# Performance work log

Hardware: AMD Instinct MI355X
Metric: run time of the kernel (lower is better)

Reference implementation:

```python
import jax, jax.numpy as jnp
import numpy as np

B = 2
NUM_CLS = 20
NUM_DIM = 256
H = W = 448
FH = FW = 28
K_TOP = 25


def _l2norm(x, eps=1e-12):
    # matches torch F.normalize(dim=1): x / max(||x||, eps); zero rows stay zero
    return x / jnp.maximum(jnp.linalg.norm(x, axis=-1, keepdims=True), eps)


def setup_inputs():
    key = jax.random.key(0)
    k1, k2, k3, k4 = jax.random.split(key, 4)
    fmap = jax.random.normal(k1, (B, NUM_DIM, FH, FW), jnp.float32)
    cam = jax.random.uniform(k2, (B, NUM_CLS, H, W), jnp.float32)
    cls_label = jax.random.randint(k3, (B, NUM_CLS), 0, 2).astype(jnp.float32)
    proj_weight = jax.random.normal(k4, (NUM_CLS, NUM_DIM), jnp.float32) * 0.02
    feature_contrast = jnp.zeros((NUM_CLS, NUM_DIM), jnp.float32)
    return {"fmap": fmap, "cam": cam, "cls_label": cls_label,
            "proj_weight": proj_weight, "feature_contrast": feature_contrast,
            "hig_thre": 0.7, "low_thre": 0.25, "bg_thre": 0.5}


def _forward(fmap, cam, cls_label, proj_weight, feature_contrast, hig_thre, low_thre, bg_thre):
    b, c, h, w = cam.shape
    d = fmap.shape[1]
    dt = fmap.dtype

    # ---- pseudo-label generation (vectorized over b,h,w) ----
    valid_cam = cls_label[:, :, None, None] * cam                       # [B,C,H,W]
    top2_v, top2_i = jax.lax.top_k(jnp.moveaxis(valid_cam, 1, -1), 2)   # [B,H,W,2]
    top1, second = top2_v[..., 0], top2_v[..., 1]
    pseudo = top2_i[..., 0] + 1
    pseudo = jnp.where(top1 < hig_thre, 255, pseudo)
    pseudo = jnp.where(top1 < low_thre, 0, pseudo)
    pseudo = jnp.where(top1 < bg_thre, 0, pseudo)
    pseudo = jnp.where((top1 - second < 0.3) & (top1 > hig_thre), 255, pseudo)

    # ---- upsample features (bilinear, align_corners=False) ----
    fmap_up = jax.image.resize(fmap, (b, d, h, w), 'bilinear')
    fmap_flat = fmap_up.reshape(b, d, h * w)                            # [B,D,HW]
    pseudo_flat = pseudo.reshape(b, h * w)                              # [B,HW]

    # ---- per-class features, both branches computed densely then selected ----
    cls_ids = jnp.arange(c) + 1
    mask = (pseudo_flat[:, None, :] == cls_ids[None, :, None]).astype(dt)  # [B,C,HW]
    counts = mask.sum(-1)                                                  # [B,C]
    feat_mask = jnp.einsum('bcp,bdp->bcd', mask, fmap_flat) / jnp.maximum(counts, 1.0)[:, :, None]
    _, top_idx = jax.lax.top_k(valid_cam.reshape(b, c, h * w), K_TOP)      # [B,C,25]
    gathered = jnp.take_along_axis(fmap_flat[:, None, :, :], top_idx[:, :, None, :], axis=-1)  # [B,C,D,25]
    feat_topk = gathered.mean(-1)                                          # [B,C,D]
    present = cls_label > 0.5                                              # [B,C] bool
    fsm = jnp.where((counts == 0.0)[:, :, None], feat_topk, feat_mask) * present[:, :, None]

    eye_f = jnp.eye(c, dtype=dt)
    eye_b = jnp.eye(c, dtype=bool)

    # ---- sequential per-sample loop (EMA memory bank carried across batch) ----
    def step(carry, xs):
        fc, loss_cls, loss_ccf = carry
        fsm_i, present_i = xs                                    # [C,D], [C]
        fsm_n = _l2norm(fsm_i)
        fc_n = _l2norm(jax.lax.stop_gradient(fc))
        cos = jnp.clip(jnp.abs(fsm_n @ fc_n.T), 1e-5, 1.0 - 1e-5)  # [C,C]
        ident = jnp.diag(present_i.astype(dt))
        loss_ccf = loss_ccf - (ident * jnp.log(cos) + (1.0 - ident) * jnp.log1p(-cos)).mean()
        off_max = jnp.where(eye_b, -jnp.inf, cos).max(axis=1)      # max over j != c
        qualify = present_i & (off_max < 0.6)                      # [C] bool
        p = jax.nn.softmax(fsm_i @ proj_weight.T, axis=-1)         # [C,C]
        logp = jnp.maximum(jnp.log(p), -100.0)
        log1mp = jnp.maximum(jnp.log1p(-p), -100.0)
        term = -(eye_f * logp + (1.0 - eye_f) * log1mp).mean(axis=-1)  # BCE(softmax, onehot) per class
        loss_cls = loss_cls + jnp.sum(jnp.where(qualify, term, 0.0))
        n = qualify.sum().astype(dt)
        loss_cls = jnp.where(n > 0, loss_cls / jnp.maximum(n, 1.0), loss_cls)
        fc = jnp.where(qualify[:, None], 0.95 * fc + 0.05 * jax.lax.stop_gradient(fsm_i), fc)
        return (fc, loss_cls, loss_ccf), None

    zero = jnp.asarray(0.0, dt)
    (_, loss_cls, loss_ccf), _ = jax.lax.scan(step, (feature_contrast, zero, zero), (fsm, present))
    return loss_ccf + loss_cls


def reference(fmap, cam, cls_label, proj_weight, feature_contrast, hig_thre, low_thre, bg_thre):
    return _forward(fmap, cam, cls_label, proj_weight, feature_contrast, hig_thre, low_thre, bg_thre)
```

## Files before the change

kernel.cpp:

```cpp
#include <hip/hip_runtime.h>
#include <cstdint>

#define HW 200704
#define IMG_W 448
#define NCLS 20
#define NDIM 256
#define NB2 784
#define LK 260

#define ASYNC_COPY4(gp, lp)                                                    \
  __builtin_amdgcn_global_load_lds(                                            \
      (const __attribute__((address_space(1))) void*)(gp),                     \
      (__attribute__((address_space(3))) void*)(lp), 4, 0, 0)

__global__ __launch_bounds__(256) void k_front(const float* __restrict__ fmap,
                                               float* __restrict__ fmapT,
                                               const float* __restrict__ cam,
                                               const float* __restrict__ cls_label,
                                               const float* __restrict__ hig_p,
                                               const float* __restrict__ low_p,
                                               const float* __restrict__ bg_p,
                                               float* __restrict__ W) {
  __shared__ float sT[NCLS][256];
  int tid = threadIdx.x;

  if (blockIdx.x >= 2 * NB2) {
    float (*tile)[33] = (float (*)[33]) & sT[0][0];
    int blk = blockIdx.x - 2 * NB2;
    int b = blk / 200;
    int t = blk % 200;
    int dT = t / 25, sT2 = t % 25;
    int ty = tid >> 5, tx = tid & 31;
#pragma unroll
    for (int r = 0; r < 4; ++r) {
      int d = dT * 32 + ty + r * 8;
      int s = sT2 * 32 + tx;
      if (s < 784) tile[ty + r * 8][tx] = fmap[((size_t)(b * 256 + d)) * 784 + s];
    }
    __syncthreads();
#pragma unroll
    for (int r = 0; r < 4; ++r) {
      int s = sT2 * 32 + ty + r * 8;
      int d = dT * 32 + tx;
      if (s < 784) fmapT[((size_t)(b * 784 + s)) * 256 + d] = tile[tx][ty + r * 8];
    }
    return;
  }

  int b = blockIdx.x / NB2;
  int blkInB = blockIdx.x % NB2;
  int pix0 = blkInB * 256;
  int wave = tid >> 6, lane = tid & 63;

  bool pres = (lane < NCLS) && (cls_label[b * NCLS + lane] != 0.0f);
  unsigned long long pm = __ballot(pres);
  unsigned mask = (unsigned)(pm & 0xFFFFFu);
  int np = __popc(mask);
  const float* camb = cam + (size_t)b * NCLS * HW + pix0 + wave * 64 + lane;

  {
    unsigned m = mask;
    for (int k = 0; k < np; ++k) {
      int c = __builtin_ctz(m); m &= m - 1u;
      ASYNC_COPY4(camb + (size_t)c * HW, &sT[k][wave * 64]);
    }
  }
  __builtin_amdgcn_s_waitcnt(0);

  float top1 = -1.0f, sec = -1.0f;
  int cls1 = 0;
  {
    unsigned m = mask;
    for (int k = 0; k < np; ++k) {
      int c = __builtin_ctz(m); m &= m - 1u;
      float x = sT[k][tid];
      bool gt = x > top1;
      sec = gt ? top1 : fmaxf(sec, fminf(x, top1));
      cls1 = gt ? c : cls1;
      top1 = gt ? x : top1;
    }
  }
  if (np < NCLS) sec = fmaxf(sec, 0.0f);
  float hig = hig_p[0], low = low_p[0], bg = bg_p[0];
  int pix = pix0 + tid;
  int ps = cls1 + 1;
  if (top1 < hig) ps = 255;
  if (top1 < low) ps = 0;
  if (top1 < bg)  ps = 0;
  if ((top1 - sec < 0.3f) && (top1 > hig)) ps = 255;
  if (ps >= 1 && ps <= NCLS) {
    int cls = ps - 1;
    int y = pix / IMG_W, x = pix % IMG_W;
    float sy = (y + 0.5f) * 0.0625f - 0.5f; sy = fminf(fmaxf(sy, 0.0f), 27.0f);
    float sx = (x + 0.5f) * 0.0625f - 0.5f; sx = fminf(fmaxf(sx, 0.0f), 27.0f);
    int fy0 = (int)sy, fx0 = (int)sx;
    int fy1 = min(fy0 + 1, 27), fx1 = min(fx0 + 1, 27);
    float wy = sy - (float)fy0, wx = sx - (float)fx0;
    float* Wb = W + (size_t)(b * NCLS + cls) * 784;
    atomicAdd(&Wb[fy0 * 28 + fx0], (1.0f - wy) * (1.0f - wx));
    atomicAdd(&Wb[fy0 * 28 + fx1], (1.0f - wy) * wx);
    atomicAdd(&Wb[fy1 * 28 + fx0], wy * (1.0f - wx));
    atomicAdd(&Wb[fy1 * 28 + fx1], wy * wx);
  }
}

__global__ __launch_bounds__(512) void k_feat(const float* __restrict__ fmapT,
                                              const float* __restrict__ cam,
                                              const float* __restrict__ Wg,
                                              const float* __restrict__ cls_label,
                                              float* __restrict__ P,
                                              float* __restrict__ S,
                                              float* __restrict__ cntW) {
  __shared__ float sW[784];
  __shared__ float sH[2][256];
  __shared__ float sRed[8];
  __shared__ float sCntf;
  __shared__ float wv[8]; __shared__ int wi[8];
  __shared__ float selV; __shared__ int selI;
  __shared__ int sTop[25];
  int bc = blockIdx.x >> 2, part = blockIdx.x & 3;
  int b = bc / NCLS;
  int tid = threadIdx.x;
  int dim = tid & 255, h = tid >> 8;
  if (cls_label[bc] == 0.0f) return;

  for (int s = tid; s < 784; s += 512) sW[s] = Wg[(size_t)bc * 784 + s];
  __syncthreads();
  {
    float cs = sW[tid >= 512 ? 0 : tid];
    cs = (tid < 512) ? sW[tid] : 0.0f;
    if (tid < 272) cs += sW[tid + 512];
    for (int off = 32; off > 0; off >>= 1) cs += __shfl_xor(cs, off, 64);
    if ((tid & 63) == 0) sRed[tid >> 6] = cs;
    __syncthreads();
    if (tid == 0) {
      float s = 0.0f;
      for (int w = 0; w < 8; ++w) s += sRed[w];
      sCntf = s;
    }
    __syncthreads();
  }
  float cntf = sCntf;
  const float* fT = fmapT + (size_t)b * 784 * 256;

  if (cntf > 0.0f) {
    int s0 = part * 196;
    if (h == 0) {
      float a0 = 0.0f, a1 = 0.0f;
      for (int s = s0; s < s0 + 196; s += 4) {
        a0 += sW[s]     * fT[(size_t)(s)     * 256 + dim];
        a1 += sW[s + 1] * fT[(size_t)(s + 1) * 256 + dim];
      }
      sH[0][dim] = a0 + a1;
    } else {
      float a2 = 0.0f, a3 = 0.0f;
      for (int s = s0; s < s0 + 196; s += 4) {
        a2 += sW[s + 2] * fT[(size_t)(s + 2) * 256 + dim];
        a3 += sW[s + 3] * fT[(size_t)(s + 3) * 256 + dim];
      }
      sH[1][dim] = a2 + a3;
    }
    __syncthreads();
    if (tid < 256)
      P[(size_t)(bc * 4 + part) * 256 + tid] = sH[0][tid] + sH[1][tid];
    if (part == 0 && tid == 0) cntW[bc] = cntf;
  } else if (part == 0) {
    if (tid == 0) cntW[bc] = 0.0f;
    const float* camc = cam + (size_t)bc * HW;
    float lastV = 3.0e38f; int lastI = -1;
    for (int r = 0; r < 25; ++r) {
      float bv = -1.0e30f; int bi = 0x7fffffff;
      for (int p = tid; p < HW; p += 512) {
        float vv2 = camc[p];
        if (((vv2 < lastV) || (vv2 == lastV && p > lastI)) &&
            ((vv2 > bv) || (vv2 == bv && p < bi))) { bv = vv2; bi = p; }
      }
      for (int off = 32; off > 0; off >>= 1) {
        float ov = __shfl_xor(bv, off, 64);
        int   oi = __shfl_xor(bi, off, 64);
        if (ov > bv || (ov == bv && oi < bi)) { bv = ov; bi = oi; }
      }
      if ((tid & 63) == 0) { wv[tid >> 6] = bv; wi[tid >> 6] = bi; }
      __syncthreads();
      if (tid == 0) {
        for (int w = 1; w < 8; ++w)
          if (wv[w] > bv || (wv[w] == bv && wi[w] < bi)) { bv = wv[w]; bi = wi[w]; }
        selV = bv; selI = bi; sTop[r] = bi;
      }
      __syncthreads();
      lastV = selV; lastI = selI;
    }
    if (tid < 256) {
      float at = 0.0f;
      for (int r = 0; r < 25; ++r) {
        int p = sTop[r];
        int y = p / IMG_W, x = p % IMG_W;
        float sy = (y + 0.5f) * 0.0625f - 0.5f; sy = fminf(fmaxf(sy, 0.0f), 27.0f);
        float sx = (x + 0.5f) * 0.0625f - 0.5f; sx = fminf(fmaxf(sx, 0.0f), 27.0f);
        int fy0 = (int)sy, fx0 = (int)sx;
        int fy1 = min(fy0 + 1, 27), fx1 = min(fx0 + 1, 27);
        float wy = sy - (float)fy0, wx = sx - (float)fx0;
        at += (1.0f - wy) * (1.0f - wx) * fT[(size_t)(fy0 * 28 + fx0) * 256 + tid]
            + (1.0f - wy) * wx          * fT[(size_t)(fy0 * 28 + fx1) * 256 + tid]
            + wy          * (1.0f - wx) * fT[(size_t)(fy1 * 28 + fx0) * 256 + tid]
            + wy          * wx          * fT[(size_t)(fy1 * 28 + fx1) * 256 + tid];
      }
      S[(size_t)bc * 256 + tid] = at * (1.0f / 25.0f);
    }
  }
}

__global__ __launch_bounds__(256) void k_pre(const float* __restrict__ P,
                                             const float* __restrict__ S,
                                             const float* __restrict__ cntW,
                                             const float* __restrict__ cls_label,
                                             const float* __restrict__ proj_w,
                                             const float* __restrict__ fc_init,
                                             float* __restrict__ BCEg,
                                             float* __restrict__ COS0,
                                             float* __restrict__ COS1V) {
  __shared__ float sOwn[LK];
  __shared__ float sFc[NCLS * LK], sPw[NCLS * LK];
  __shared__ float sF0[NCLS * LK], sFv[NCLS * LK];
  __shared__ float sLog[NCLS];
  __shared__ float sNC[NCLS], sNCv[NCLS];
  __shared__ int   sZC[NCLS], sZCv[NCLS];
  __shared__ float sNI[1]; __shared__ int sZI[1];
  int tid = threadIdx.x;
  int b = blockIdx.x / NCLS, i = blockIdx.x % NCLS;

  for (int idx = tid; idx < NCLS * NDIM; idx += 256) {
    int r = idx >> 8, d = idx & 255;
    sFc[r * LK + d] = fc_init[idx];
    sPw[r * LK + d] = proj_w[idx];
  }
  {
    int bc = b * NCLS + i, d = tid;
    float v = 0.0f;
    if (cls_label[bc] != 0.0f) {
      float c = cntW[bc];
      if (c > 0.0f) {
        const float* p = P + (size_t)bc * 1024 + d;
        v = ((p[0] + p[256]) + (p[512] + p[768])) / fmaxf(c, 1.0f);
      } else {
        v = S[(size_t)bc * 256 + d];
      }
    }
    sOwn[d] = v;
  }
  if (b == 1) {
    for (int idx = tid; idx < NCLS * NDIM; idx += 256) {
      int bc = idx >> 8, d = idx & 255;
      float v = 0.0f;
      if (cls_label[bc] != 0.0f) {
        float c = cntW[bc];
        if (c > 0.0f) {
          const float* p = P + (size_t)bc * 1024 + d;
          v = ((p[0] + p[256]) + (p[512] + p[768])) / fmaxf(c, 1.0f);
        } else {
          v = S[(size_t)bc * 256 + d];
        }
      }
      sF0[bc * LK + d] = v;
    }
  }
  __syncthreads();
  if (b == 1) {
    for (int idx = tid; idx < NCLS * NDIM; idx += 256) {
      int r = idx >> 8, d = idx & 255;
      sFv[r * LK + d] = 0.95f * sFc[r * LK + d] + 0.05f * sF0[r * LK + d];
    }
    __syncthreads();
  }

  {
    int g = tid >> 3, sub = tid & 7;
    if (g <= 20) {
      const float* row = (g < 20) ? &sFc[g * LK] : sOwn;
      float a0 = 0.0f, a1 = 0.0f, a2 = 0.0f, a3 = 0.0f;
      int d0 = sub * 32;
#pragma unroll
      for (int d = d0; d < d0 + 32; d += 8) {
        float4 x = *(const float4*)&row[d];
        float4 y = *(const float4*)&row[d + 4];
        a0 += x.x * x.x + x.y * x.y;
        a1 += x.z * x.z + x.w * x.w;
        a2 += y.x * y.x + y.y * y.y;
        a3 += y.z * y.z + y.w * y.w;
      }
      float s = (a0 + a1) + (a2 + a3);
      s += __shfl_xor(s, 1, 64);
      s += __shfl_xor(s, 2, 64);
      s += __shfl_xor(s, 4, 64);
      if (sub == 0) {
        if (g < 20) { sNC[g] = fmaxf(sqrtf(s), 1e-12f); sZC[g] = (s == 0.0f); }
        else        { sNI[0] = fmaxf(sqrtf(s), 1e-12f); sZI[0] = (s == 0.0f); }
      }
    }
  }
  __syncthreads();
  if (b == 1) {
    int g = tid >> 3, sub = tid & 7;
    if (g < 20) {
      const float* row = &sFv[g * LK];
      float a0 = 0.0f, a1 = 0.0f, a2 = 0.0f, a3 = 0.0f;
      int d0 = sub * 32;
#pragma unroll
      for (int d = d0; d < d0 + 32; d += 8) {
        float4 x = *(const float4*)&row[d];
        float4 y = *(const float4*)&row[d + 4];
        a0 += x.x * x.x + x.y * x.y;
        a1 += x.z * x.z + x.w * x.w;
        a2 += y.x * y.x + y.y * y.y;
        a3 += y.z * y.z + y.w * y.w;
      }
      float s = (a0 + a1) + (a2 + a3);
      s += __shfl_xor(s, 1, 64);
      s += __shfl_xor(s, 2, 64);
      s += __shfl_xor(s, 4, 64);
      if (sub == 0) { sNCv[g] = fmaxf(sqrtf(s), 1e-12f); sZCv[g] = (s == 0.0f); }
    }
    __syncthreads();
  }

  if (tid < NCLS) {
    const float* ra = sOwn;
    const float* rb = &sPw[tid * LK];
    float a0 = 0, a1 = 0, a2 = 0, a3 = 0, a4 = 0, a5 = 0, a6 = 0, a7 = 0;
    for (int d = 0; d < 256; d += 16) {
      float4 x0 = *(const float4*)&ra[d],      y0 = *(const float4*)&rb[d];
      float4 x1 = *(const float4*)&ra[d + 4],  y1 = *(const float4*)&rb[d + 4];
      float4 x2 = *(const float4*)&ra[d + 8],  y2 = *(const float4*)&rb[d + 8];
      float4 x3 = *(const float4*)&ra[d + 12], y3 = *(const float4*)&rb[d + 12];
      a0 += x0.x * y0.x + x0.y * y0.y;  a1 += x0.z * y0.z + x0.w * y0.w;
      a2 += x1.x * y1.x + x1.y * y1.y;  a3 += x1.z * y1.z + x1.w * y1.w;
      a4 += x2.x * y2.x + x2.y * y2.y;  a5 += x2.z * y2.z + x2.w * y2.w;
      a6 += x3.x * y3.x + x3.y * y3.y;  a7 += x3.z * y3.z + x3.w * y3.w;
    }
    sLog[tid] = ((a0 + a1) + (a2 + a3)) + ((a4 + a5) + (a6 + a7));
  }
  __syncthreads();

  if (tid < 32) {
    int jj = tid;
    float l = (jj < NCLS) ? sLog[jj] : -3.0e38f;
    float m = l;
#pragma unroll
    for (int off = 1; off < 32; off <<= 1) m = fmaxf(m, __shfl_xor(m, off, 64));
    float e = (jj < NCLS) ? expf(l - m) : 0.0f;
    float sS = e;
#pragma unroll
    for (int off = 1; off < 32; off <<= 1) sS += __shfl_xor(sS, off, 64);
    float term = 0.0f;
    if (jj < NCLS) {
      float p = e / sS;
      term = (jj == i) ? fmaxf(logf(p), -100.0f) : fmaxf(log1pf(-p), -100.0f);
    }
#pragma unroll
    for (int off = 1; off < 32; off <<= 1) term += __shfl_xor(term, off, 64);
    if (jj == 0) BCEg[b * NCLS + i] = -term / 20.0f;
  }
  if (tid >= 64 && tid < 64 + 2 * NCLS) {
    int j = (tid - 64) >> 1, sub = tid & 1;
    float c0;
    if (sZI[0] || sZC[j]) c0 = 0.0f;
    else {
      const float* ra = sOwn;
      const float* rb = &sFc[j * LK];
      float a0 = 0.0f, a1 = 0.0f, a2 = 0.0f, a3 = 0.0f;
      int d0 = sub * 128;
      for (int d = d0; d < d0 + 128; d += 8) {
        float4 x  = *(const float4*)&ra[d];
        float4 y  = *(const float4*)&rb[d];
        float4 x2 = *(const float4*)&ra[d + 4];
        float4 y2 = *(const float4*)&rb[d + 4];
        a0 += x.x * y.x + x.y * y.y;
        a1 += x.z * y.z + x.w * y.w;
        a2 += x2.x * y2.x + x2.y * y2.y;
        a3 += x2.z * y2.z + x2.w * y2.w;
      }
      float acc = (a0 + a1) + (a2 + a3);
      acc += __shfl_xor(acc, 1, 64);
      c0 = fabsf(acc / (sNI[0] * sNC[j]));
    }
    if (sub == 0) {
      float cv = fminf(fmaxf(c0, 1e-5f), 1.0f - 1e-5f);
      if (b == 0) COS0[i * NCLS + j] = cv;
      else        COS1V[i * NCLS + j] = cv;
    }
  }
  if (b == 1 && tid >= 128 && tid < 128 + 2 * NCLS) {
    int j = (tid - 128) >> 1, sub = tid & 1;
    float c0;
    if (sZI[0] || sZCv[j]) c0 = 0.0f;
    else {
      const float* ra = sOwn;
      const float* rb = &sFv[j * LK];
      float a0 = 0.0f, a1 = 0.0f, a2 = 0.0f, a3 = 0.0f;
      int d0 = sub * 128;
      for (int d = d0; d < d0 + 128; d += 8) {
        float4 x  = *(const float4*)&ra[d];
        float4 y  = *(const float4*)&rb[d];
        float4 x2 = *(const float4*)&ra[d + 4];
        float4 y2 = *(const float4*)&rb[d + 4];
        a0 += x.x * y.x + x.y * y.y;
        a1 += x.z * y.z + x.w * y.w;
        a2 += x2.x * y2.x + x2.y * y2.y;
        a3 += x2.z * y2.z + x2.w * y2.w;
      }
      float acc = (a0 + a1) + (a2 + a3);
      acc += __shfl_xor(acc, 1, 64);
      c0 = fabsf(acc / (sNI[0] * sNCv[j]));
    }
    if (sub == 0)
      COS1V[400 + i * NCLS + j] = fminf(fmaxf(c0, 1e-5f), 1.0f - 1e-5f);
  }
}

__global__ __launch_bounds__(1024) void k_final(const float* __restrict__ BCEg,
                                                const float* __restrict__ COS0,
                                                const float* __restrict__ COS1V,
                                                const float* __restrict__ cls_label,
                                                float* __restrict__ out) {
  __shared__ float sCos[400];
  __shared__ float sBCE[2][NCLS], sRow[NCLS];
  __shared__ int   sQual[NCLS];
  __shared__ float sPres[2][NCLS];
  __shared__ float sScal[2];
  int tid = threadIdx.x;

  if (tid < 400) sCos[tid] = COS0[tid];
  if (tid < 40) { sBCE[tid / NCLS][tid % NCLS] = BCEg[tid];
                  sPres[tid / NCLS][tid % NCLS] = cls_label[tid]; }
  if (tid == 0) { sScal[0] = 0.0f; sScal[1] = 0.0f; }
  __syncthreads();

  for (int b = 0; b < 2; ++b) {
    if (b == 1) {
      if (tid < 400) {
        int j = tid % NCLS;
        sCos[tid] = sQual[j] ? COS1V[400 + tid] : COS1V[tid];
      }
      __syncthreads();
    }
    {
      int i = tid >> 5, jj = tid & 31;
      if (i < NCLS) {
        float pres = (sPres[b][i] > 0.5f) ? 1.0f : 0.0f;
        float contrib = 0.0f, omv = -3.0e38f;
        if (jj < NCLS) {
          float c0 = sCos[i * NCLS + jj];
          float ident = (jj == i) ? pres : 0.0f;
          contrib = ident * logf(c0) + (1.0f - ident) * log1pf(-c0);
          if (jj != i) omv = c0;
        }
#pragma unroll
        for (int off = 1; off < 32; off <<= 1) {
          contrib += __shfl_xor(contrib, off, 64);
          omv = fmaxf(omv, __shfl_xor(omv, off, 64));
        }
        if (jj == 0) { sRow[i] = contrib; sQual[i] = (pres > 0.5f && omv < 0.6f) ? 1 : 0; }
      }
    }
    __syncthreads();
    if (tid == 0) {
      float s = 0.0f;
      for (int r = 0; r < NCLS; ++r) s += sRow[r];
      sScal[0] -= s / 400.0f;
      float add = 0.0f; int nq = 0;
      for (int r = 0; r < NCLS; ++r) if (sQual[r]) { add += sBCE[b][r]; nq++; }
      float lc = sScal[1] + add;
      if (nq > 0) lc = lc / fmaxf((float)nq, 1.0f);
      sScal[1] = lc;
    }
    __syncthreads();
  }
  if (tid == 0) out[0] = sScal[0] + sScal[1];
}

extern "C" void kernel_launch(void* const* d_in, const int* in_sizes, int n_in,
                              void* d_out, int out_size, void* d_ws, size_t ws_size,
                              hipStream_t stream) {
  const float* fmap      = (const float*)d_in[0];
  const float* cam       = (const float*)d_in[1];
  const float* cls_label = (const float*)d_in[2];
  const float* proj_w    = (const float*)d_in[3];
  const float* fc_init   = (const float*)d_in[4];
  const float* hig       = (const float*)d_in[5];
  const float* low       = (const float*)d_in[6];
  const float* bg        = (const float*)d_in[7];
  float* out = (float*)d_out;

  char* ws = (char*)d_ws;
  float* W     = (float*)(ws);
  float* cntW  = (float*)(ws + 125440);
  float* P     = (float*)(ws + 125600);
  float* S     = (float*)(ws + 289440);
  float* fmapT = (float*)(ws + 330400);
  float* BCEg  = (float*)(ws + 1936032);
  float* COS0v = (float*)(ws + 1936192);
  float* COS1V = (float*)(ws + 1937792);

  hipMemsetAsync(ws, 0, 125440, stream);
  k_front<<<2 * NB2 + 400,  256, 0, stream>>>(fmap, fmapT, cam, cls_label,
                                              hig, low, bg, W);
  k_feat <<<          160,  512, 0, stream>>>(fmapT, cam, W, cls_label, P, S, cntW);
  k_pre  <<<   2 * NCLS,    256, 0, stream>>>(P, S, cntW, cls_label, proj_w,
                                              fc_init, BCEg, COS0v, COS1V);
  k_final<<<            1, 1024, 0, stream>>>(BCEg, COS0v, COS1V, cls_label, out);
}
```

Measured before the change: 121.0 us.

## Merge feature, pre and final kernels into one launch with atomic tickets

Fuses k_feat, k_pre and k_final into a single 200-block kernel. The last 40 blocks preload their constant tables, then spin on an atomic ticket counter until the 160 feature blocks finish. The final reduction runs in whichever pre block increments the second ticket last. This removes two kernel launches and their inter-kernel gaps. It depends on all 200 blocks being co-resident, since a waiting block would otherwise deadlock, and the pre blocks now use 512 threads, which raises their shared-memory and register footprint.

```diff
diff --git a/kernel.cpp b/kernel.cpp
--- a/kernel.cpp
+++ b/kernel.cpp
@@ -104,121 +104,127 @@
   }
 }
 
-__global__ __launch_bounds__(512) void k_feat(const float* __restrict__ fmapT,
-                                              const float* __restrict__ cam,
-                                              const float* __restrict__ Wg,
-                                              const float* __restrict__ cls_label,
-                                              float* __restrict__ P,
-                                              float* __restrict__ S,
-                                              float* __restrict__ cntW) {
-  __shared__ float sW[784];
-  __shared__ float sH[2][256];
-  __shared__ float sRed[8];
-  __shared__ float sCntf;
-  __shared__ float wv[8]; __shared__ int wi[8];
-  __shared__ float selV; __shared__ int selI;
-  __shared__ int sTop[25];
-  int bc = blockIdx.x >> 2, part = blockIdx.x & 3;
-  int b = bc / NCLS;
-  int tid = threadIdx.x;
-  int dim = tid & 255, h = tid >> 8;
-  if (cls_label[bc] == 0.0f) return;
-
-  for (int s = tid; s < 784; s += 512) sW[s] = Wg[(size_t)bc * 784 + s];
-  __syncthreads();
-  {
-    float cs = sW[tid >= 512 ? 0 : tid];
-    cs = (tid < 512) ? sW[tid] : 0.0f;
-    if (tid < 272) cs += sW[tid + 512];
-    for (int off = 32; off > 0; off >>= 1) cs += __shfl_xor(cs, off, 64);
-    if ((tid & 63) == 0) sRed[tid >> 6] = cs;
-    __syncthreads();
-    if (tid == 0) {
-      float s = 0.0f;
-      for (int w = 0; w < 8; ++w) s += sRed[w];
-      sCntf = s;
-    }
-    __syncthreads();
-  }
-  float cntf = sCntf;
-  const float* fT = fmapT + (size_t)b * 784 * 256;
-
-  if (cntf > 0.0f) {
-    int s0 = part * 196;
-    if (h == 0) {
-      float a0 = 0.0f, a1 = 0.0f;
-      for (int s = s0; s < s0 + 196; s += 4) {
-        a0 += sW[s]     * fT[(size_t)(s)     * 256 + dim];
-        a1 += sW[s + 1] * fT[(size_t)(s + 1) * 256 + dim];
-      }
-      sH[0][dim] = a0 + a1;
-    } else {
-      float a2 = 0.0f, a3 = 0.0f;
-      for (int s = s0; s < s0 + 196; s += 4) {
-        a2 += sW[s + 2] * fT[(size_t)(s + 2) * 256 + dim];
-        a3 += sW[s + 3] * fT[(size_t)(s + 3) * 256 + dim];
-      }
-      sH[1][dim] = a2 + a3;
-    }
-    __syncthreads();
-    if (tid < 256)
-      P[(size_t)(bc * 4 + part) * 256 + tid] = sH[0][tid] + sH[1][tid];
-    if (part == 0 && tid == 0) cntW[bc] = cntf;
-  } else if (part == 0) {
-    if (tid == 0) cntW[bc] = 0.0f;
-    const float* camc = cam + (size_t)bc * HW;
-    float lastV = 3.0e38f; int lastI = -1;
-    for (int r = 0; r < 25; ++r) {
-      float bv = -1.0e30f; int bi = 0x7fffffff;
-      for (int p = tid; p < HW; p += 512) {
-        float vv2 = camc[p];
-        if (((vv2 < lastV) || (vv2 == lastV && p > lastI)) &&
-            ((vv2 > bv) || (vv2 == bv && p < bi))) { bv = vv2; bi = p; }
-      }
-      for (int off = 32; off > 0; off >>= 1) {
-        float ov = __shfl_xor(bv, off, 64);
-        int   oi = __shfl_xor(bi, off, 64);
-        if (ov > bv || (ov == bv && oi < bi)) { bv = ov; bi = oi; }
-      }
-      if ((tid & 63) == 0) { wv[tid >> 6] = bv; wi[tid >> 6] = bi; }
-      __syncthreads();
-      if (tid == 0) {
-        for (int w = 1; w < 8; ++w)
-          if (wv[w] > bv || (wv[w] == bv && wi[w] < bi)) { bv = wv[w]; bi = wi[w]; }
-        selV = bv; selI = bi; sTop[r] = bi;
-      }
-      __syncthreads();
-      lastV = selV; lastI = selI;
-    }
-    if (tid < 256) {
-      float at = 0.0f;
-      for (int r = 0; r < 25; ++r) {
-        int p = sTop[r];
-        int y = p / IMG_W, x = p % IMG_W;
-        float sy = (y + 0.5f) * 0.0625f - 0.5f; sy = fminf(fmaxf(sy, 0.0f), 27.0f);
-        float sx = (x + 0.5f) * 0.0625f - 0.5f; sx = fminf(fmaxf(sx, 0.0f), 27.0f);
-        int fy0 = (int)sy, fx0 = (int)sx;
-        int fy1 = min(fy0 + 1, 27), fx1 = min(fx0 + 1, 27);
-        float wy = sy - (float)fy0, wx = sx - (float)fx0;
-        at += (1.0f - wy) * (1.0f - wx) * fT[(size_t)(fy0 * 28 + fx0) * 256 + tid]
-            + (1.0f - wy) * wx          * fT[(size_t)(fy0 * 28 + fx1) * 256 + tid]
-            + wy          * (1.0f - wx) * fT[(size_t)(fy1 * 28 + fx0) * 256 + tid]
-            + wy          * wx          * fT[(size_t)(fy1 * 28 + fx1) * 256 + tid];
-      }
-      S[(size_t)bc * 256 + tid] = at * (1.0f / 25.0f);
-    }
-  }
-}
-
-__global__ __launch_bounds__(256) void k_pre(const float* __restrict__ P,
-                                             const float* __restrict__ S,
-                                             const float* __restrict__ cntW,
+__global__ __launch_bounds__(512) void k_mid(const float* __restrict__ fmapT,
+                                             const float* __restrict__ cam,
+                                             const float* __restrict__ Wg,
                                              const float* __restrict__ cls_label,
+                                             float* __restrict__ P,
+                                             float* __restrict__ S,
+                                             float* __restrict__ cntW,
                                              const float* __restrict__ proj_w,
                                              const float* __restrict__ fc_init,
                                              float* __restrict__ BCEg,
                                              float* __restrict__ COS0,
-                                             float* __restrict__ COS1V) {
+                                             float* __restrict__ COS1V,
+                                             unsigned* tickets,
+                                             float* __restrict__ out) {
+  int tid = threadIdx.x;
+
+  if (blockIdx.x < 160) {
+    __shared__ float sW[784];
+    __shared__ float sH[2][256];
+    __shared__ float sRed[8];
+    __shared__ float sCntf;
+    __shared__ float wv[8]; __shared__ int wi[8];
+    __shared__ float selV; __shared__ int selI;
+    __shared__ int sTop[25];
+    int bc = blockIdx.x >> 2, part = blockIdx.x & 3;
+    int b = bc / NCLS;
+    int dim = tid & 255, h = tid >> 8;
+
+    if (cls_label[bc] != 0.0f) {
+      for (int s = tid; s < 784; s += 512) sW[s] = Wg[(size_t)bc * 784 + s];
+      __syncthreads();
+      {
+        float cs = sW[tid >= 512 ? 0 : tid];
+        cs = (tid < 512) ? sW[tid] : 0.0f;
+        if (tid < 272) cs += sW[tid + 512];
+        for (int off = 32; off > 0; off >>= 1) cs += __shfl_xor(cs, off, 64);
+        if ((tid & 63) == 0) sRed[tid >> 6] = cs;
+        __syncthreads();
+        if (tid == 0) {
+          float s = 0.0f;
+          for (int w = 0; w < 8; ++w) s += sRed[w];
+          sCntf = s;
+        }
+        __syncthreads();
+      }
+      float cntf = sCntf;
+      const float* fT = fmapT + (size_t)b * 784 * 256;
+
+      if (cntf > 0.0f) {
+        int s0 = part * 196;
+        if (h == 0) {
+          float a0 = 0.0f, a1 = 0.0f;
+          for (int s = s0; s < s0 + 196; s += 4) {
+            a0 += sW[s]     * fT[(size_t)(s)     * 256 + dim];
+            a1 += sW[s + 1] * fT[(size_t)(s + 1) * 256 + dim];
+          }
+          sH[0][dim] = a0 + a1;
+        } else {
+          float a2 = 0.0f, a3 = 0.0f;
+          for (int s = s0; s < s0 + 196; s += 4) {
+            a2 += sW[s + 2] * fT[(size_t)(s + 2) * 256 + dim];
+            a3 += sW[s + 3] * fT[(size_t)(s + 3) * 256 + dim];
+          }
+          sH[1][dim] = a2 + a3;
+        }
+        __syncthreads();
+        if (tid < 256)
+          P[(size_t)(bc * 4 + part) * 256 + tid] = sH[0][tid] + sH[1][tid];
+        if (part == 0 && tid == 0) cntW[bc] = cntf;
+      } else if (part == 0) {
+        if (tid == 0) cntW[bc] = 0.0f;
+        const float* camc = cam + (size_t)bc * HW;
+        float lastV = 3.0e38f; int lastI = -1;
+        for (int r = 0; r < 25; ++r) {
+          float bv = -1.0e30f; int bi = 0x7fffffff;
+          for (int p = tid; p < HW; p += 512) {
+            float vv2 = camc[p];
+            if (((vv2 < lastV) || (vv2 == lastV && p > lastI)) &&
+                ((vv2 > bv) || (vv2 == bv && p < bi))) { bv = vv2; bi = p; }
+          }
+          for (int off = 32; off > 0; off >>= 1) {
+            float ov = __shfl_xor(bv, off, 64);
+            int   oi = __shfl_xor(bi, off, 64);
+            if (ov > bv || (ov == bv && oi < bi)) { bv = ov; bi = oi; }
+          }
+          if ((tid & 63) == 0) { wv[tid >> 6] = bv; wi[tid >> 6] = bi; }
+          __syncthreads();
+          if (tid == 0) {
+            for (int w = 1; w < 8; ++w)
+              if (wv[w] > bv || (wv[w] == bv && wi[w] < bi)) { bv = wv[w]; bi = wi[w]; }
+            selV = bv; selI = bi; sTop[r] = bi;
+          }
+          __syncthreads();
+          lastV = selV; lastI = selI;
+        }
+        if (tid < 256) {
+          float at = 0.0f;
+          for (int r = 0; r < 25; ++r) {
+            int p = sTop[r];
+            int y = p / IMG_W, x = p % IMG_W;
+            float sy = (y + 0.5f) * 0.0625f - 0.5f; sy = fminf(fmaxf(sy, 0.0f), 27.0f);
+            float sx = (x + 0.5f) * 0.0625f - 0.5f; sx = fminf(fmaxf(sx, 0.0f), 27.0f);
+            int fy0 = (int)sy, fx0 = (int)sx;
+            int fy1 = min(fy0 + 1, 27), fx1 = min(fx0 + 1, 27);
+            float wy = sy - (float)fy0, wx = sx - (float)fx0;
+            at += (1.0f - wy) * (1.0f - wx) * fT[(size_t)(fy0 * 28 + fx0) * 256 + tid]
+                + (1.0f - wy) * wx          * fT[(size_t)(fy0 * 28 + fx1) * 256 + tid]
+                + wy          * (1.0f - wx) * fT[(size_t)(fy1 * 28 + fx0) * 256 + tid]
+                + wy          * wx          * fT[(size_t)(fy1 * 28 + fx1) * 256 + tid];
+          }
+          S[(size_t)bc * 256 + tid] = at * (1.0f / 25.0f);
+        }
+      }
+    }
+    __syncthreads();
+    if (tid == 0) { __threadfence(); atomicAdd(tickets, 1u); }
+    return;
+  }
+
+  int bp = blockIdx.x - 160;
+  int b = bp / NCLS, i = bp % NCLS;
   __shared__ float sOwn[LK];
   __shared__ float sFc[NCLS * LK], sPw[NCLS * LK];
   __shared__ float sF0[NCLS * LK], sFv[NCLS * LK];
@@ -226,15 +232,27 @@
   __shared__ float sNC[NCLS], sNCv[NCLS];
   __shared__ int   sZC[NCLS], sZCv[NCLS];
   __shared__ float sNI[1]; __shared__ int sZI[1];
-  int tid = threadIdx.x;
-  int b = blockIdx.x / NCLS, i = blockIdx.x % NCLS;
-
-  for (int idx = tid; idx < NCLS * NDIM; idx += 256) {
+  __shared__ float sCos[400];
+  __shared__ float sBCE[2][NCLS], sRow[NCLS];
+  __shared__ int   sQual[NCLS];
+  __shared__ float sPres[2][NCLS];
+  __shared__ float sScal[2];
+  __shared__ unsigned sLast;
+
+  for (int idx = tid; idx < NCLS * NDIM; idx += 512) {
     int r = idx >> 8, d = idx & 255;
     sFc[r * LK + d] = fc_init[idx];
     sPw[r * LK + d] = proj_w[idx];
   }
-  {
+
+  if (tid == 0) {
+    while (__hip_atomic_load(tickets, __ATOMIC_ACQUIRE, __HIP_MEMORY_SCOPE_AGENT) < 160u)
+      __builtin_amdgcn_s_sleep(4);
+  }
+  __syncthreads();
+  __threadfence();
+
+  if (tid < 256) {
     int bc = b * NCLS + i, d = tid;
     float v = 0.0f;
     if (cls_label[bc] != 0.0f) {
@@ -249,7 +267,7 @@
     sOwn[d] = v;
   }
   if (b == 1) {
-    for (int idx = tid; idx < NCLS * NDIM; idx += 256) {
+    for (int idx = tid; idx < NCLS * NDIM; idx += 512) {
       int bc = idx >> 8, d = idx & 255;
       float v = 0.0f;
       if (cls_label[bc] != 0.0f) {
@@ -266,7 +284,7 @@
   }
   __syncthreads();
   if (b == 1) {
-    for (int idx = tid; idx < NCLS * NDIM; idx += 256) {
+    for (int idx = tid; idx < NCLS * NDIM; idx += 512) {
       int r = idx >> 8, d = idx & 255;
       sFv[r * LK + d] = 0.95f * sFc[r * LK + d] + 0.05f * sF0[r * LK + d];
     }
@@ -415,19 +433,12 @@
     if (sub == 0)
       COS1V[400 + i * NCLS + j] = fminf(fmaxf(c0, 1e-5f), 1.0f - 1e-5f);
   }
-}
-
-__global__ __launch_bounds__(1024) void k_final(const float* __restrict__ BCEg,
-                                                const float* __restrict__ COS0,
-                                                const float* __restrict__ COS1V,
-                                                const float* __restrict__ cls_label,
-                                                float* __restrict__ out) {
-  __shared__ float sCos[400];
-  __shared__ float sBCE[2][NCLS], sRow[NCLS];
-  __shared__ int   sQual[NCLS];
-  __shared__ float sPres[2][NCLS];
-  __shared__ float sScal[2];
-  int tid = threadIdx.x;
+
+  __syncthreads();
+  if (tid == 0) { __threadfence(); sLast = atomicAdd(tickets + 1, 1u); }
+  __syncthreads();
+  if (sLast != 39u) return;
+  __threadfence();
 
   if (tid < 400) sCos[tid] = COS0[tid];
   if (tid < 40) { sBCE[tid / NCLS][tid % NCLS] = BCEg[tid];
@@ -435,8 +446,8 @@
   if (tid == 0) { sScal[0] = 0.0f; sScal[1] = 0.0f; }
   __syncthreads();
 
-  for (int b = 0; b < 2; ++b) {
-    if (b == 1) {
+  for (int bb = 0; bb < 2; ++bb) {
+    if (bb == 1) {
       if (tid < 400) {
         int j = tid % NCLS;
         sCos[tid] = sQual[j] ? COS1V[400 + tid] : COS1V[tid];
@@ -444,22 +455,22 @@
       __syncthreads();
     }
     {
-      int i = tid >> 5, jj = tid & 31;
-      if (i < NCLS) {
-        float pres = (sPres[b][i] > 0.5f) ? 1.0f : 0.0f;
+      int jj = tid & 31;
+      for (int r = tid >> 5; r < NCLS; r += 16) {
+        float pres = (sPres[bb][r] > 0.5f) ? 1.0f : 0.0f;
         float contrib = 0.0f, omv = -3.0e38f;
         if (jj < NCLS) {
-          float c0 = sCos[i * NCLS + jj];
-          float ident = (jj == i) ? pres : 0.0f;
+          float c0 = sCos[r * NCLS + jj];
+          float ident = (jj == r) ? pres : 0.0f;
           contrib = ident * logf(c0) + (1.0f - ident) * log1pf(-c0);
-          if (jj != i) omv = c0;
+          if (jj != r) omv = c0;
         }
 #pragma unroll
         for (int off = 1; off < 32; off <<= 1) {
           contrib += __shfl_xor(contrib, off, 64);
           omv = fmaxf(omv, __shfl_xor(omv, off, 64));
         }
-        if (jj == 0) { sRow[i] = contrib; sQual[i] = (pres > 0.5f && omv < 0.6f) ? 1 : 0; }
+        if (jj == 0) { sRow[r] = contrib; sQual[r] = (pres > 0.5f && omv < 0.6f) ? 1 : 0; }
       }
     }
     __syncthreads();
@@ -468,7 +479,7 @@
       for (int r = 0; r < NCLS; ++r) s += sRow[r];
       sScal[0] -= s / 400.0f;
       float add = 0.0f; int nq = 0;
-      for (int r = 0; r < NCLS; ++r) if (sQual[r]) { add += sBCE[b][r]; nq++; }
+      for (int r = 0; r < NCLS; ++r) if (sQual[r]) { add += sBCE[bb][r]; nq++; }
       float lc = sScal[1] + add;
       if (nq > 0) lc = lc / fmaxf((float)nq, 1.0f);
       sScal[1] = lc;
@@ -492,20 +503,20 @@
   float* out = (float*)d_out;
 
   char* ws = (char*)d_ws;
-  float* W     = (float*)(ws);
-  float* cntW  = (float*)(ws + 125440);
-  float* P     = (float*)(ws + 125600);
-  float* S     = (float*)(ws + 289440);
-  float* fmapT = (float*)(ws + 330400);
-  float* BCEg  = (float*)(ws + 1936032);
-  float* COS0v = (float*)(ws + 1936192);
-  float* COS1V = (float*)(ws + 1937792);
-
-  hipMemsetAsync(ws, 0, 125440, stream);
-  k_front<<<2 * NB2 + 400,  256, 0, stream>>>(fmap, fmapT, cam, cls_label,
-                                              hig, low, bg, W);
-  k_feat <<<          160,  512, 0, stream>>>(fmapT, cam, W, cls_label, P, S, cntW);
-  k_pre  <<<   2 * NCLS,    256, 0, stream>>>(P, S, cntW, cls_label, proj_w,
-                                              fc_init, BCEg, COS0v, COS1V);
-  k_final<<<            1, 1024, 0, stream>>>(BCEg, COS0v, COS1V, cls_label, out);
+  float*    W     = (float*)(ws);
+  unsigned* tick  = (unsigned*)(ws + 125440);
+  float*    cntW  = (float*)(ws + 125456);
+  float*    P     = (float*)(ws + 125616);
+  float*    S     = (float*)(ws + 289456);
+  float*    fmapT = (float*)(ws + 330416);
+  float*    BCEg  = (float*)(ws + 1936048);
+  float*    COS0  = (float*)(ws + 1936208);
+  float*    COS1V = (float*)(ws + 1937808);
+
+  hipMemsetAsync(ws, 0, 125456, stream);
+  k_front<<<2 * NB2 + 400, 256, 0, stream>>>(fmap, fmapT, cam, cls_label,
+                                             hig, low, bg, W);
+  k_mid  <<<          200, 512, 0, stream>>>(fmapT, cam, W, cls_label, P, S,
+                                             cntW, proj_w, fc_init, BCEg,
+                                             COS0, COS1V, tick, out);
 }
```

New measurement: 128.1 us. 1.06x slower.
